# Kernel optimization log

Hardware: AMD Instinct MI355X
Metric: run time of the kernel (lower is better)

Reference implementation:

```python
import jax, jax.numpy as jnp
import numpy as np

INPUT, HIDDEN, OUTPUT = 256, 512, 64
B, T = 128, 256

def gru_layer(x, W_ih, W_hh, b_ih, b_hh):
    # x: [B, T, in]; W_ih: [3H, in]; W_hh: [3H, H]; gate order r, z, n (PyTorch)
    Bv = x.shape[0]
    H = W_hh.shape[1]
    xg = jnp.einsum('bti,gi->btg', x, W_ih) + b_ih  # precompute input gates [B,T,3H]

    def step(h, xg_t):
        hg = h @ W_hh.T + b_hh
        xr, xz, xn = jnp.split(xg_t, 3, axis=-1)
        hr, hz, hn = jnp.split(hg, 3, axis=-1)
        r = jax.nn.sigmoid(xr + hr)
        z = jax.nn.sigmoid(xz + hz)
        n = jnp.tanh(xn + r * hn)
        h_new = (1.0 - z) * n + z * h
        return h_new, h_new

    h0 = jnp.zeros((Bv, H), x.dtype)
    _, ys = jax.lax.scan(step, h0, jnp.swapaxes(xg, 0, 1))  # [T,B,H]
    return jnp.swapaxes(ys, 0, 1)  # [B,T,H]

def setup_inputs() -> dict:
    key = jax.random.key(0)
    ks = jax.random.split(key, 12)
    s_in = 1.0 / np.sqrt(HIDDEN)
    inp = {
        'x': jax.random.normal(ks[0], (B, T, INPUT), dtype=jnp.float32),
        'W_ih0': jax.random.uniform(ks[1], (3 * HIDDEN, INPUT), minval=-s_in, maxval=s_in),
        'W_hh0': jax.random.uniform(ks[2], (3 * HIDDEN, HIDDEN), minval=-s_in, maxval=s_in),
        'b_ih0': jax.random.uniform(ks[3], (3 * HIDDEN,), minval=-s_in, maxval=s_in),
        'b_hh0': jax.random.uniform(ks[4], (3 * HIDDEN,), minval=-s_in, maxval=s_in),
        'W_ih1': jax.random.uniform(ks[5], (3 * HIDDEN, HIDDEN), minval=-s_in, maxval=s_in),
        'W_hh1': jax.random.uniform(ks[6], (3 * HIDDEN, HIDDEN), minval=-s_in, maxval=s_in),
        'b_ih1': jax.random.uniform(ks[7], (3 * HIDDEN,), minval=-s_in, maxval=s_in),
        'b_hh1': jax.random.uniform(ks[8], (3 * HIDDEN,), minval=-s_in, maxval=s_in),
        'W_out': jax.random.uniform(ks[9], (OUTPUT, HIDDEN), minval=-s_in, maxval=s_in),
        'b_out': jax.random.uniform(ks[10], (OUTPUT,), minval=-s_in, maxval=s_in),
    }
    return inp

def reference(x, W_ih0, W_hh0, b_ih0, b_hh0, W_ih1, W_hh1, b_ih1, b_hh1, W_out, b_out):
    h = gru_layer(x, W_ih0, W_hh0, b_ih0, b_hh0)   # layer 0
    h = gru_layer(h, W_ih1, W_hh1, b_ih1, b_hh1)   # layer 1 (dropout=0.0 -> no-op)
    last = h[:, -1, :]                              # [B, H]
    yhat = last @ W_out.T + b_out                   # [B, OUTPUT]
    return yhat
```

## Files before the change

kernel.cpp:

```cpp
#include <hip/hip_runtime.h>
#include <hip/hip_bf16.h>
#include <stdint.h>

typedef __attribute__((ext_vector_type(8))) __bf16 bf16x8;
typedef __attribute__((ext_vector_type(4))) float  floatx4;

#define T_STEPS 256
#define BATCH   128
#define HID     512

__device__ __forceinline__ float sigmoidf_(float x) { return 1.f / (1.f + __expf(-x)); }
__device__ __forceinline__ float tanhf_(float y) {
  float e = __expf(-2.f * fabsf(y));
  return copysignf((1.f - e) / (1.f + e), y);
}

template <int SLP>
__device__ __forceinline__ void pollline_(const int* base, int target) {
  while (1) {
    int v = __hip_atomic_load(base, __ATOMIC_RELAXED, __HIP_MEMORY_SCOPE_AGENT);
    if (__all(v >= target)) break;
    __builtin_amdgcn_s_sleep(SLP);
  }
  asm volatile("" ::: "memory");
}

__global__ __launch_bounds__(256) void gru_fused(
    const float* __restrict__ x,
    const float* __restrict__ Wih0, const float* __restrict__ Whh0,
    const float* __restrict__ bih0, const float* __restrict__ bhh0,
    const float* __restrict__ Wih1, const float* __restrict__ Whh1,
    const float* __restrict__ bih1, const float* __restrict__ bhh1,
    __bf16* __restrict__ h0base,
    __bf16* __restrict__ h1base,
    int* __restrict__ fl)
{
  const int tid   = threadIdx.x;
  const int layer = blockIdx.x >> 7;
  const int bg    = (blockIdx.x >> 6) & 1;
  const int g     = blockIdx.x & 63;
  const int w = tid >> 6, l = tid & 63, c = l & 15, q = l >> 4;
  const int Kin = layer ? HID : 256;
  const int KTx = Kin >> 5;
  const int KT  = KTx + 16;
  const int rowbase = bg * 64 + w * 16;
  const int jj  = g * 8 + c;

  const float* Wih = layer ? Wih1 : Wih0;
  const float* Whh = layer ? Whh1 : Whh0;
  const float* bih = layer ? bih1 : bih0;
  const float* bhh = layer ? bhh1 : bhh0;
  __bf16* hbase = layer ? h1base : h0base;

  __shared__ __bf16 ldsW[2 * 32 * 64 * 8];

  for (int cid = tid; cid < 2 * KT * 64; cid += 256) {
    int nt = cid / (KT * 64);
    int r1 = cid - nt * (KT * 64);
    int kt = r1 >> 6;
    int ll = r1 & 63;
    int cc = ll & 15, qq = ll >> 4;
    int k  = kt * 32 + qq * 8;
    int grow;
    if (nt == 0) grow = (cc < 8) ? (g * 8 + cc) : (512 + g * 8 + (cc - 8));
    else         grow = (cc < 8) ? (1024 + g * 8 + cc) : -1;
    bf16x8 v;
    if (grow >= 0) {
      const float* src = (k < Kin) ? (Wih + (size_t)grow * Kin + k)
                                   : (Whh + (size_t)grow * HID + (k - Kin));
      #pragma unroll
      for (int j = 0; j < 8; ++j) v[j] = (__bf16)src[j];
    } else {
      #pragma unroll
      for (int j = 0; j < 8; ++j) v[j] = (__bf16)0.f;
    }
    *(bf16x8*)&ldsW[((size_t)(nt * KT + kt) * 64 + ll) * 8] = v;
  }
  __syncthreads();

  bf16x8 WH[16][2];
  #pragma unroll
  for (int kt = 0; kt < 16; ++kt) {
    WH[kt][0] = *(const bf16x8*)&ldsW[((size_t)(0 * KT + KTx + kt) * 64 + l) * 8];
    WH[kt][1] = *(const bf16x8*)&ldsW[((size_t)(1 * KT + KTx + kt) * 64 + l) * 8];
  }

  float bias0, bias_nx, bias_nh;
  if (c < 8) {
    bias0   = bih[jj] + bhh[jj];
    bias_nx = bih[1024 + jj];
    bias_nh = bhh[1024 + jj];
  } else {
    int j2 = g * 8 + (c - 8);
    bias0   = bih[512 + j2] + bhh[512 + j2];
    bias_nx = 0.f; bias_nh = 0.f;
  }

  floatx4 accA[2], accB[2];
  const floatx4 zero4 = {0.f, 0.f, 0.f, 0.f};
  float hprev[4] = {0.f, 0.f, 0.f, 0.f};

  int* fpost      = fl + ((size_t)((layer * 2 + bg) * 64 + g)) * 32;
  const int* fown = fl + ((size_t)((layer * 2 + bg) * 64 + l)) * 32;
  const int* fx   = fl + ((size_t)(bg * 64 + l)) * 32;

  auto hslab = [&](int t) -> __bf16* {
    return hbase + (size_t)t * (BATCH * HID);
  };

  auto phaseX = [&](int t) {
    accA[0] = zero4; accA[1] = zero4;
    if (layer == 0) {
      const float* xp = x + ((size_t)(rowbase + c) * T_STEPS + t) * 256 + q * 8;
      for (int kt = 0; kt < 8; ++kt) {
        bf16x8 b0 = *(const bf16x8*)&ldsW[((size_t)(0 * KT + kt) * 64 + l) * 8];
        bf16x8 b1 = *(const bf16x8*)&ldsW[((size_t)(1 * KT + kt) * 64 + l) * 8];
        floatx4 u = *(const floatx4*)(xp + kt * 32);
        floatx4 v = *(const floatx4*)(xp + kt * 32 + 4);
        bf16x8 a;
        a[0] = (__bf16)u[0]; a[1] = (__bf16)u[1]; a[2] = (__bf16)u[2]; a[3] = (__bf16)u[3];
        a[4] = (__bf16)v[0]; a[5] = (__bf16)v[1]; a[6] = (__bf16)v[2]; a[7] = (__bf16)v[3];
        accA[0] = __builtin_amdgcn_mfma_f32_16x16x32_bf16(a, b0, accA[0], 0, 0, 0);
        accA[1] = __builtin_amdgcn_mfma_f32_16x16x32_bf16(a, b1, accA[1], 0, 0, 0);
      }
    } else {
      const __bf16* xp = h0base + (size_t)t * (BATCH * HID)
                       + (size_t)(rowbase + c) * HID + q * 8;
      for (int kt = 0; kt < 16; ++kt) {
        bf16x8 b0 = *(const bf16x8*)&ldsW[((size_t)(0 * KT + kt) * 64 + l) * 8];
        bf16x8 b1 = *(const bf16x8*)&ldsW[((size_t)(1 * KT + kt) * 64 + l) * 8];
        bf16x8 a = *(const bf16x8*)(xp + kt * 32);
        accA[0] = __builtin_amdgcn_mfma_f32_16x16x32_bf16(a, b0, accA[0], 0, 0, 0);
        accA[1] = __builtin_amdgcn_mfma_f32_16x16x32_bf16(a, b1, accA[1], 0, 0, 0);
      }
    }
  };

  if (layer == 1) pollline_<2>(fx, 1);
  phaseX(0);

  for (int t = 0; t < T_STEPS; ++t) {
    accB[0] = zero4; accB[1] = zero4;
    if (t > 0) {
      const __bf16* hA = hslab(t - 1) + (size_t)(rowbase + c) * HID + q * 8;
      bf16x8 hfrag[16];
      #pragma unroll
      for (int kt = 0; kt < 16; ++kt)
        hfrag[kt] = *(const bf16x8*)(hA + kt * 32);
      #pragma unroll
      for (int kt = 0; kt < 16; ++kt) {
        accB[0] = __builtin_amdgcn_mfma_f32_16x16x32_bf16(hfrag[kt], WH[kt][0], accB[0], 0, 0, 0);
        accB[1] = __builtin_amdgcn_mfma_f32_16x16x32_bf16(hfrag[kt], WH[kt][1], accB[1], 0, 0, 0);
      }
    }

    __bf16* hs = hslab(t);
    #pragma unroll
    for (int rg = 0; rg < 4; ++rg) {
      float pre0 = accA[0][rg] + accB[0][rg] + bias0;
      float zs = __shfl(pre0, (l & 48) | ((c + 8) & 15), 64);
      float r  = sigmoidf_(pre0);
      float z  = sigmoidf_(zs);
      float nn = tanhf_(accA[1][rg] + bias_nx + r * (accB[1][rg] + bias_nh));
      float hnew = (1.f - z) * nn + z * hprev[rg];
      hprev[rg] = hnew;
      unsigned short us = __builtin_bit_cast(unsigned short, (__bf16)hnew);
      int po = __shfl_xor((int)us, 1, 64);
      if (c < 8 && (c & 1) == 0) {
        uint32_t v = (uint32_t)us | ((uint32_t)po << 16);
        int row = rowbase + q * 4 + rg;
        __hip_atomic_store((uint32_t*)(hs + (size_t)row * HID + jj), v,
                           __ATOMIC_RELAXED, __HIP_MEMORY_SCOPE_AGENT);
      }
    }

    asm volatile("s_waitcnt vmcnt(0)" ::: "memory");
    __syncthreads();
    if (tid == 0)
      __hip_atomic_store(fpost, t + 1, __ATOMIC_RELAXED, __HIP_MEMORY_SCOPE_AGENT);

    if (t + 1 < T_STEPS) {
      if (layer == 1) pollline_<2>(fx, t + 2);
      phaseX(t + 1);
      pollline_<1>(fown, t + 1);
    }
  }
}

__global__ __launch_bounds__(64) void outproj(const __bf16* __restrict__ h1,
                                              const float* __restrict__ Wout,
                                              const float* __restrict__ bout,
                                              float* __restrict__ out) {
  int b = blockIdx.x, o = threadIdx.x;
  const __bf16* hr = h1 + (size_t)b * HID;
  const float*  wr = Wout + (size_t)o * HID;
  float acc = bout[o];
  for (int k = 0; k < HID; k += 8) {
    bf16x8 h8 = *(const bf16x8*)(hr + k);
    #pragma unroll
    for (int j = 0; j < 8; ++j) acc += (float)h8[j] * wr[k + j];
  }
  out[b * 64 + o] = acc;
}

extern "C" void kernel_launch(void* const* d_in, const int* in_sizes, int n_in,
                              void* d_out, int out_size, void* d_ws, size_t ws_size,
                              hipStream_t stream) {
  const float* x    = (const float*)d_in[0];
  const float* Wih0 = (const float*)d_in[1];
  const float* Whh0 = (const float*)d_in[2];
  const float* bih0 = (const float*)d_in[3];
  const float* bhh0 = (const float*)d_in[4];
  const float* Wih1 = (const float*)d_in[5];
  const float* Whh1 = (const float*)d_in[6];
  const float* bih1 = (const float*)d_in[7];
  const float* bhh1 = (const float*)d_in[8];
  const float* Wout = (const float*)d_in[9];
  const float* bout = (const float*)d_in[10];

  char* ws = (char*)d_ws;
  __bf16* h0 = (__bf16*)(ws);
  __bf16* h1 = (__bf16*)(ws + (32u << 20));
  int*    fl = (int*)(ws + (64u << 20));

  (void)hipMemsetAsync(fl, 0, 2 * 2 * 64 * 32 * 4, stream);

  gru_fused<<<256, 256, 0, stream>>>(x,
                                     Wih0, Whh0, bih0, bhh0,
                                     Wih1, Whh1, bih1, bhh1,
                                     h0, h1, fl);

  outproj<<<128, 64, 0, stream>>>(h1 + (size_t)255 * BATCH * HID,
                                  Wout, bout, (float*)d_out);
}
```

Measured before the change: 1.707 ms.

## Replace flag-based step sync with sentinel-polled hidden-state loads

Drops the per-block flag counters, the per-step __syncthreads and the flag poll/post. The h workspace is pre-filled with a sentinel pattern, and consumers spin on cache-bypassing dwordx4 loads of the h slab until no dword still holds the sentinel. Producer-to-consumer latency now comes straight from the data, with no separate barrier and flag round trip. In exchange, every launch must memset 64 MB of workspace, and polling puts more load traffic on the memory system.

```diff
diff --git a/kernel.cpp b/kernel.cpp
--- a/kernel.cpp
+++ b/kernel.cpp
@@ -4,10 +4,12 @@
 
 typedef __attribute__((ext_vector_type(8))) __bf16 bf16x8;
 typedef __attribute__((ext_vector_type(4))) float  floatx4;
+typedef __attribute__((ext_vector_type(4))) unsigned int uintx4;
 
 #define T_STEPS 256
 #define BATCH   128
 #define HID     512
+#define SENTW 0x7F7F7F7Fu
 
 __device__ __forceinline__ float sigmoidf_(float x) { return 1.f / (1.f + __expf(-x)); }
 __device__ __forceinline__ float tanhf_(float y) {
@@ -15,14 +17,32 @@
   return copysignf((1.f - e) / (1.f + e), y);
 }
 
-template <int SLP>
-__device__ __forceinline__ void pollline_(const int* base, int target) {
-  while (1) {
-    int v = __hip_atomic_load(base, __ATOMIC_RELAXED, __HIP_MEMORY_SCOPE_AGENT);
-    if (__all(v >= target)) break;
-    __builtin_amdgcn_s_sleep(SLP);
-  }
-  asm volatile("" ::: "memory");
+__device__ __forceinline__ bool okw_(uintx4 w) {
+  return (w[0] != SENTW) & (w[1] != SENTW) & (w[2] != SENTW) & (w[3] != SENTW);
+}
+
+__device__ __forceinline__ void sentload16_(const __bf16* base, uintx4* hw) {
+  unsigned pend = 0xFFFFu;
+  while (pend) {
+    #pragma unroll
+    for (int kt = 0; kt < 16; ++kt)
+      if (pend & (1u << kt)) {
+        const void* p = (const void*)(base + kt * 32);
+        asm volatile("global_load_dwordx4 %0, %1, off sc0 sc1"
+                     : "=v"(hw[kt]) : "v"(p));
+      }
+    asm volatile("s_waitcnt vmcnt(0)" ::: "memory");
+    __builtin_amdgcn_sched_barrier(0);
+    unsigned np = 0;
+    #pragma unroll
+    for (int kt = 0; kt < 16; ++kt)
+      if (pend & (1u << kt)) {
+        if (!okw_(hw[kt])) np |= (1u << kt);
+      }
+    pend = np;
+    if (pend == 0xFFFFu) __builtin_amdgcn_s_sleep(4);
+    else if (pend)       __builtin_amdgcn_s_sleep(1);
+  }
 }
 
 __global__ __launch_bounds__(256) void gru_fused(
@@ -32,8 +52,7 @@
     const float* __restrict__ Wih1, const float* __restrict__ Whh1,
     const float* __restrict__ bih1, const float* __restrict__ bhh1,
     __bf16* __restrict__ h0base,
-    __bf16* __restrict__ h1base,
-    int* __restrict__ fl)
+    __bf16* __restrict__ h1base)
 {
   const int tid   = threadIdx.x;
   const int layer = blockIdx.x >> 7;
@@ -100,10 +119,6 @@
   const floatx4 zero4 = {0.f, 0.f, 0.f, 0.f};
   float hprev[4] = {0.f, 0.f, 0.f, 0.f};
 
-  int* fpost      = fl + ((size_t)((layer * 2 + bg) * 64 + g)) * 32;
-  const int* fown = fl + ((size_t)((layer * 2 + bg) * 64 + l)) * 32;
-  const int* fx   = fl + ((size_t)(bg * 64 + l)) * 32;
-
   auto hslab = [&](int t) -> __bf16* {
     return hbase + (size_t)t * (BATCH * HID);
   };
@@ -126,31 +141,32 @@
     } else {
       const __bf16* xp = h0base + (size_t)t * (BATCH * HID)
                        + (size_t)(rowbase + c) * HID + q * 8;
+      uintx4 aw[16];
+      sentload16_(xp, aw);
+      #pragma unroll
       for (int kt = 0; kt < 16; ++kt) {
         bf16x8 b0 = *(const bf16x8*)&ldsW[((size_t)(0 * KT + kt) * 64 + l) * 8];
         bf16x8 b1 = *(const bf16x8*)&ldsW[((size_t)(1 * KT + kt) * 64 + l) * 8];
-        bf16x8 a = *(const bf16x8*)(xp + kt * 32);
+        bf16x8 a  = __builtin_bit_cast(bf16x8, aw[kt]);
         accA[0] = __builtin_amdgcn_mfma_f32_16x16x32_bf16(a, b0, accA[0], 0, 0, 0);
         accA[1] = __builtin_amdgcn_mfma_f32_16x16x32_bf16(a, b1, accA[1], 0, 0, 0);
       }
     }
   };
 
-  if (layer == 1) pollline_<2>(fx, 1);
   phaseX(0);
 
   for (int t = 0; t < T_STEPS; ++t) {
     accB[0] = zero4; accB[1] = zero4;
     if (t > 0) {
       const __bf16* hA = hslab(t - 1) + (size_t)(rowbase + c) * HID + q * 8;
-      bf16x8 hfrag[16];
-      #pragma unroll
-      for (int kt = 0; kt < 16; ++kt)
-        hfrag[kt] = *(const bf16x8*)(hA + kt * 32);
+      uintx4 hw[16];
+      sentload16_(hA, hw);
       #pragma unroll
       for (int kt = 0; kt < 16; ++kt) {
-        accB[0] = __builtin_amdgcn_mfma_f32_16x16x32_bf16(hfrag[kt], WH[kt][0], accB[0], 0, 0, 0);
-        accB[1] = __builtin_amdgcn_mfma_f32_16x16x32_bf16(hfrag[kt], WH[kt][1], accB[1], 0, 0, 0);
+        bf16x8 hf = __builtin_bit_cast(bf16x8, hw[kt]);
+        accB[0] = __builtin_amdgcn_mfma_f32_16x16x32_bf16(hf, WH[kt][0], accB[0], 0, 0, 0);
+        accB[1] = __builtin_amdgcn_mfma_f32_16x16x32_bf16(hf, WH[kt][1], accB[1], 0, 0, 0);
       }
     }
 
@@ -174,16 +190,7 @@
       }
     }
 
-    asm volatile("s_waitcnt vmcnt(0)" ::: "memory");
-    __syncthreads();
-    if (tid == 0)
-      __hip_atomic_store(fpost, t + 1, __ATOMIC_RELAXED, __HIP_MEMORY_SCOPE_AGENT);
-
-    if (t + 1 < T_STEPS) {
-      if (layer == 1) pollline_<2>(fx, t + 2);
-      phaseX(t + 1);
-      pollline_<1>(fown, t + 1);
-    }
+    if (t + 1 < T_STEPS) phaseX(t + 1);
   }
 }
 
@@ -221,14 +228,13 @@
   char* ws = (char*)d_ws;
   __bf16* h0 = (__bf16*)(ws);
   __bf16* h1 = (__bf16*)(ws + (32u << 20));
-  int*    fl = (int*)(ws + (64u << 20));
-
-  (void)hipMemsetAsync(fl, 0, 2 * 2 * 64 * 32 * 4, stream);
+
+  (void)hipMemsetAsync(ws, 0x7F, (64u << 20), stream);
 
   gru_fused<<<256, 256, 0, stream>>>(x,
                                      Wih0, Whh0, bih0, bhh0,
                                      Wih1, Whh1, bih1, bhh1,
-                                     h0, h1, fl);
+                                     h0, h1);
 
   outproj<<<128, 64, 0, stream>>>(h1 + (size_t)255 * BATCH * HID,
                                   Wout, bout, (float*)d_out);
```

New measurement: 1.716 ms. No clear change (+0.5%).

## Repartition GRU blocks to 16 hidden units per block with full r,z,n tiles

Applied to the files above, without the earlier changes.

Each block now owns 16 hidden columns for all three gates (r, z, n), with 4 batch groups of 32 rows and 128 threads per block, instead of 8 columns per block with r and z packed into one tile over 64 rows. This removes the zero-padded MFMA tile and the cross-lane shuffle for z, and halves the number of blocks per batch group that each wait polls (32 flags instead of 64). In exchange each wave holds 48 register-resident W_hh fragments and issues three MFMA chains per step, which raises register pressure. With fewer waves per block, per-step latency may also grow.

```diff
diff --git a/kernel.cpp b/kernel.cpp
--- a/kernel.cpp
+++ b/kernel.cpp
@@ -16,16 +16,17 @@
 }
 
 template <int SLP>
-__device__ __forceinline__ void pollline_(const int* base, int target) {
+__device__ __forceinline__ void pollring_(const int* base, int target) {
+  const int* p = base + (size_t)(threadIdx.x & 31) * 32;
   while (1) {
-    int v = __hip_atomic_load(base, __ATOMIC_RELAXED, __HIP_MEMORY_SCOPE_AGENT);
+    int v = __hip_atomic_load(p, __ATOMIC_RELAXED, __HIP_MEMORY_SCOPE_AGENT);
     if (__all(v >= target)) break;
     __builtin_amdgcn_s_sleep(SLP);
   }
   asm volatile("" ::: "memory");
 }
 
-__global__ __launch_bounds__(256) void gru_fused(
+__global__ __launch_bounds__(128, 1) void gru_fused(
     const float* __restrict__ x,
     const float* __restrict__ Wih0, const float* __restrict__ Whh0,
     const float* __restrict__ bih0, const float* __restrict__ bhh0,
@@ -37,14 +38,14 @@
 {
   const int tid   = threadIdx.x;
   const int layer = blockIdx.x >> 7;
-  const int bg    = (blockIdx.x >> 6) & 1;
-  const int g     = blockIdx.x & 63;
+  const int bg    = (blockIdx.x >> 5) & 3;
+  const int g     = blockIdx.x & 31;
   const int w = tid >> 6, l = tid & 63, c = l & 15, q = l >> 4;
   const int Kin = layer ? HID : 256;
   const int KTx = Kin >> 5;
   const int KT  = KTx + 16;
-  const int rowbase = bg * 64 + w * 16;
-  const int jj  = g * 8 + c;
+  const int rowbase = bg * 32 + w * 16;
+  const int jj  = g * 16 + c;
 
   const float* Wih = layer ? Wih1 : Wih0;
   const float* Whh = layer ? Whh1 : Whh0;
@@ -52,69 +53,58 @@
   const float* bhh = layer ? bhh1 : bhh0;
   __bf16* hbase = layer ? h1base : h0base;
 
-  __shared__ __bf16 ldsW[2 * 32 * 64 * 8];
-
-  for (int cid = tid; cid < 2 * KT * 64; cid += 256) {
+  __shared__ __bf16 ldsW[3 * 32 * 64 * 8];
+
+  for (int cid = tid; cid < 3 * KT * 64; cid += 128) {
     int nt = cid / (KT * 64);
     int r1 = cid - nt * (KT * 64);
     int kt = r1 >> 6;
     int ll = r1 & 63;
     int cc = ll & 15, qq = ll >> 4;
     int k  = kt * 32 + qq * 8;
-    int grow;
-    if (nt == 0) grow = (cc < 8) ? (g * 8 + cc) : (512 + g * 8 + (cc - 8));
-    else         grow = (cc < 8) ? (1024 + g * 8 + cc) : -1;
+    int grow = nt * 512 + g * 16 + cc;
+    const float* src = (k < Kin) ? (Wih + (size_t)grow * Kin + k)
+                                 : (Whh + (size_t)grow * HID + (k - Kin));
     bf16x8 v;
-    if (grow >= 0) {
-      const float* src = (k < Kin) ? (Wih + (size_t)grow * Kin + k)
-                                   : (Whh + (size_t)grow * HID + (k - Kin));
-      #pragma unroll
-      for (int j = 0; j < 8; ++j) v[j] = (__bf16)src[j];
-    } else {
-      #pragma unroll
-      for (int j = 0; j < 8; ++j) v[j] = (__bf16)0.f;
-    }
+    #pragma unroll
+    for (int j = 0; j < 8; ++j) v[j] = (__bf16)src[j];
     *(bf16x8*)&ldsW[((size_t)(nt * KT + kt) * 64 + ll) * 8] = v;
   }
   __syncthreads();
 
-  bf16x8 WH[16][2];
+  bf16x8 WH[16][3];
   #pragma unroll
   for (int kt = 0; kt < 16; ++kt) {
     WH[kt][0] = *(const bf16x8*)&ldsW[((size_t)(0 * KT + KTx + kt) * 64 + l) * 8];
     WH[kt][1] = *(const bf16x8*)&ldsW[((size_t)(1 * KT + KTx + kt) * 64 + l) * 8];
-  }
-
-  float bias0, bias_nx, bias_nh;
-  if (c < 8) {
-    bias0   = bih[jj] + bhh[jj];
-    bias_nx = bih[1024 + jj];
-    bias_nh = bhh[1024 + jj];
-  } else {
-    int j2 = g * 8 + (c - 8);
-    bias0   = bih[512 + j2] + bhh[512 + j2];
-    bias_nx = 0.f; bias_nh = 0.f;
-  }
-
-  floatx4 accA[2], accB[2];
+    WH[kt][2] = *(const bf16x8*)&ldsW[((size_t)(2 * KT + KTx + kt) * 64 + l) * 8];
+  }
+
+  const float bias_r  = bih[jj]        + bhh[jj];
+  const float bias_z  = bih[512 + jj]  + bhh[512 + jj];
+  const float bias_nx = bih[1024 + jj];
+  const float bias_nh = bhh[1024 + jj];
+
+  floatx4 accA[3], accB[3];
   const floatx4 zero4 = {0.f, 0.f, 0.f, 0.f};
   float hprev[4] = {0.f, 0.f, 0.f, 0.f};
 
-  int* fpost      = fl + ((size_t)((layer * 2 + bg) * 64 + g)) * 32;
-  const int* fown = fl + ((size_t)((layer * 2 + bg) * 64 + l)) * 32;
-  const int* fx   = fl + ((size_t)(bg * 64 + l)) * 32;
+  int*       fpost = fl + ((size_t)((layer * 4 + bg) * 32 + g)) * 32;
+  const int* fown  = fl + ((size_t)((layer * 4 + bg) * 32)) * 32;
+  const int* fx    = fl + ((size_t)((0     * 4 + bg) * 32)) * 32;
 
   auto hslab = [&](int t) -> __bf16* {
     return hbase + (size_t)t * (BATCH * HID);
   };
 
   auto phaseX = [&](int t) {
-    accA[0] = zero4; accA[1] = zero4;
+    accA[0] = zero4; accA[1] = zero4; accA[2] = zero4;
     if (layer == 0) {
       const float* xp = x + ((size_t)(rowbase + c) * T_STEPS + t) * 256 + q * 8;
       for (int kt = 0; kt < 8; ++kt) {
         bf16x8 b0 = *(const bf16x8*)&ldsW[((size_t)(0 * KT + kt) * 64 + l) * 8];
         bf16x8 b1 = *(const bf16x8*)&ldsW[((size_t)(1 * KT + kt) * 64 + l) * 8];
+        bf16x8 b2 = *(const bf16x8*)&ldsW[((size_t)(2 * KT + kt) * 64 + l) * 8];
         floatx4 u = *(const floatx4*)(xp + kt * 32);
         floatx4 v = *(const floatx4*)(xp + kt * 32 + 4);
         bf16x8 a;
@@ -122,6 +112,7 @@
         a[4] = (__bf16)v[0]; a[5] = (__bf16)v[1]; a[6] = (__bf16)v[2]; a[7] = (__bf16)v[3];
         accA[0] = __builtin_amdgcn_mfma_f32_16x16x32_bf16(a, b0, accA[0], 0, 0, 0);
         accA[1] = __builtin_amdgcn_mfma_f32_16x16x32_bf16(a, b1, accA[1], 0, 0, 0);
+        accA[2] = __builtin_amdgcn_mfma_f32_16x16x32_bf16(a, b2, accA[2], 0, 0, 0);
       }
     } else {
       const __bf16* xp = h0base + (size_t)t * (BATCH * HID)
@@ -129,18 +120,20 @@
       for (int kt = 0; kt < 16; ++kt) {
         bf16x8 b0 = *(const bf16x8*)&ldsW[((size_t)(0 * KT + kt) * 64 + l) * 8];
         bf16x8 b1 = *(const bf16x8*)&ldsW[((size_t)(1 * KT + kt) * 64 + l) * 8];
+        bf16x8 b2 = *(const bf16x8*)&ldsW[((size_t)(2 * KT + kt) * 64 + l) * 8];
         bf16x8 a = *(const bf16x8*)(xp + kt * 32);
         accA[0] = __builtin_amdgcn_mfma_f32_16x16x32_bf16(a, b0, accA[0], 0, 0, 0);
         accA[1] = __builtin_amdgcn_mfma_f32_16x16x32_bf16(a, b1, accA[1], 0, 0, 0);
+        accA[2] = __builtin_amdgcn_mfma_f32_16x16x32_bf16(a, b2, accA[2], 0, 0, 0);
       }
     }
   };
 
-  if (layer == 1) pollline_<2>(fx, 1);
+  if (layer == 1) pollring_<2>(fx, 1);
   phaseX(0);
 
   for (int t = 0; t < T_STEPS; ++t) {
-    accB[0] = zero4; accB[1] = zero4;
+    accB[0] = zero4; accB[1] = zero4; accB[2] = zero4;
     if (t > 0) {
       const __bf16* hA = hslab(t - 1) + (size_t)(rowbase + c) * HID + q * 8;
       bf16x8 hfrag[16];
@@ -151,22 +144,21 @@
       for (int kt = 0; kt < 16; ++kt) {
         accB[0] = __builtin_amdgcn_mfma_f32_16x16x32_bf16(hfrag[kt], WH[kt][0], accB[0], 0, 0, 0);
         accB[1] = __builtin_amdgcn_mfma_f32_16x16x32_bf16(hfrag[kt], WH[kt][1], accB[1], 0, 0, 0);
+        accB[2] = __builtin_amdgcn_mfma_f32_16x16x32_bf16(hfrag[kt], WH[kt][2], accB[2], 0, 0, 0);
       }
     }
 
     __bf16* hs = hslab(t);
     #pragma unroll
     for (int rg = 0; rg < 4; ++rg) {
-      float pre0 = accA[0][rg] + accB[0][rg] + bias0;
-      float zs = __shfl(pre0, (l & 48) | ((c + 8) & 15), 64);
-      float r  = sigmoidf_(pre0);
-      float z  = sigmoidf_(zs);
-      float nn = tanhf_(accA[1][rg] + bias_nx + r * (accB[1][rg] + bias_nh));
+      float r  = sigmoidf_(accA[0][rg] + accB[0][rg] + bias_r);
+      float z  = sigmoidf_(accA[1][rg] + accB[1][rg] + bias_z);
+      float nn = tanhf_(accA[2][rg] + bias_nx + r * (accB[2][rg] + bias_nh));
       float hnew = (1.f - z) * nn + z * hprev[rg];
       hprev[rg] = hnew;
       unsigned short us = __builtin_bit_cast(unsigned short, (__bf16)hnew);
       int po = __shfl_xor((int)us, 1, 64);
-      if (c < 8 && (c & 1) == 0) {
+      if ((c & 1) == 0) {
         uint32_t v = (uint32_t)us | ((uint32_t)po << 16);
         int row = rowbase + q * 4 + rg;
         __hip_atomic_store((uint32_t*)(hs + (size_t)row * HID + jj), v,
@@ -180,9 +172,9 @@
       __hip_atomic_store(fpost, t + 1, __ATOMIC_RELAXED, __HIP_MEMORY_SCOPE_AGENT);
 
     if (t + 1 < T_STEPS) {
-      if (layer == 1) pollline_<2>(fx, t + 2);
+      if (layer == 1) pollring_<2>(fx, t + 2);
       phaseX(t + 1);
-      pollline_<1>(fown, t + 1);
+      pollring_<1>(fown, t + 1);
     }
   }
 }
@@ -223,9 +215,9 @@
   __bf16* h1 = (__bf16*)(ws + (32u << 20));
   int*    fl = (int*)(ws + (64u << 20));
 
-  (void)hipMemsetAsync(fl, 0, 2 * 2 * 64 * 32 * 4, stream);
-
-  gru_fused<<<256, 256, 0, stream>>>(x,
+  (void)hipMemsetAsync(fl, 0, 2 * 4 * 32 * 32 * 4, stream);
+
+  gru_fused<<<256, 128, 0, stream>>>(x,
                                      Wih0, Whh0, bih0, bhh0,
                                      Wih1, Whh1, bih1, bhh1,
                                      h0, h1, fl);
```

Measured after the change: 1.893 ms. +10.8%, slower.

## Use per-wave flags, packed 16-byte h stores, and drop block barrier

Applied to the files above, without the earlier changes.

Each wave now publishes its own progress flag instead of one flag per block, so the per-step __syncthreads is removed and waves only wait on the matching wave rows in other blocks. The hidden-state write is gathered by shuffles into one 16-byte store per row with sc0 sc1 cache bits, replacing four 4-byte atomic stores. Layer 1's wait on layer 0 moves before the flag post so it overlaps the store drain. This cuts barrier and store overhead on the recurrent critical path, but it relies on the per-wave flag layout being correct and on the inline-asm store being visible before the flag is posted.

```diff
diff --git a/kernel.cpp b/kernel.cpp
--- a/kernel.cpp
+++ b/kernel.cpp
@@ -4,10 +4,12 @@
 
 typedef __attribute__((ext_vector_type(8))) __bf16 bf16x8;
 typedef __attribute__((ext_vector_type(4))) float  floatx4;
+typedef __attribute__((ext_vector_type(4))) unsigned int uintx4;
 
 #define T_STEPS 256
 #define BATCH   128
 #define HID     512
+#define FLS     16
 
 __device__ __forceinline__ float sigmoidf_(float x) { return 1.f / (1.f + __expf(-x)); }
 __device__ __forceinline__ float tanhf_(float y) {
@@ -100,9 +102,9 @@
   const floatx4 zero4 = {0.f, 0.f, 0.f, 0.f};
   float hprev[4] = {0.f, 0.f, 0.f, 0.f};
 
-  int* fpost      = fl + ((size_t)((layer * 2 + bg) * 64 + g)) * 32;
-  const int* fown = fl + ((size_t)((layer * 2 + bg) * 64 + l)) * 32;
-  const int* fx   = fl + ((size_t)(bg * 64 + l)) * 32;
+  int*       fpost = fl + ((size_t)(((layer * 2 + bg) * 4 + w) * 64 + g)) * FLS;
+  const int* fown  = fl + ((size_t)(((layer * 2 + bg) * 4 + w) * 64 + l)) * FLS;
+  const int* fx    = fl + ((size_t)(((0     * 2 + bg) * 4 + w) * 64 + l)) * FLS;
 
   auto hslab = [&](int t) -> __bf16* {
     return hbase + (size_t)t * (BATCH * HID);
@@ -164,23 +166,28 @@
       float nn = tanhf_(accA[1][rg] + bias_nx + r * (accB[1][rg] + bias_nh));
       float hnew = (1.f - z) * nn + z * hprev[rg];
       hprev[rg] = hnew;
-      unsigned short us = __builtin_bit_cast(unsigned short, (__bf16)hnew);
-      int po = __shfl_xor((int)us, 1, 64);
-      if (c < 8 && (c & 1) == 0) {
-        uint32_t v = (uint32_t)us | ((uint32_t)po << 16);
+      unsigned int us = (unsigned int)__builtin_bit_cast(unsigned short, (__bf16)hnew);
+      unsigned int v01 = us | ((unsigned int)__shfl_xor((int)us, 1, 64) << 16);
+      unsigned int v23 = (unsigned int)__shfl_xor((int)v01, 2, 64);
+      unsigned int v45 = (unsigned int)__shfl_xor((int)v01, 4, 64);
+      unsigned int v67 = (unsigned int)__shfl_xor((int)v23, 4, 64);
+      if (c == 0) {
+        uintx4 pv = {v01, v23, v45, v67};
         int row = rowbase + q * 4 + rg;
-        __hip_atomic_store((uint32_t*)(hs + (size_t)row * HID + jj), v,
-                           __ATOMIC_RELAXED, __HIP_MEMORY_SCOPE_AGENT);
-      }
-    }
-
+        void* dst = (void*)(hs + (size_t)row * HID + g * 8);
+        asm volatile("global_store_dwordx4 %0, %1, off sc0 sc1"
+                     :: "v"(dst), "v"(pv) : "memory");
+      }
+    }
+
+    if (layer == 1 && t + 1 < T_STEPS) {
+      pollline_<2>(fx, t + 2);
+    }
     asm volatile("s_waitcnt vmcnt(0)" ::: "memory");
-    __syncthreads();
-    if (tid == 0)
+    if (l == 0)
       __hip_atomic_store(fpost, t + 1, __ATOMIC_RELAXED, __HIP_MEMORY_SCOPE_AGENT);
 
     if (t + 1 < T_STEPS) {
-      if (layer == 1) pollline_<2>(fx, t + 2);
       phaseX(t + 1);
       pollline_<1>(fown, t + 1);
     }
@@ -223,7 +230,7 @@
   __bf16* h1 = (__bf16*)(ws + (32u << 20));
   int*    fl = (int*)(ws + (64u << 20));
 
-  (void)hipMemsetAsync(fl, 0, 2 * 2 * 64 * 32 * 4, stream);
+  (void)hipMemsetAsync(fl, 0, 2 * 2 * 4 * 64 * FLS * 4, stream);
 
   gru_fused<<<256, 256, 0, stream>>>(x,
                                      Wih0, Whh0, bih0, bhh0,
```

Result: slower. 1.812 ms (+6.1%).
